# Performance work log

Measured on AMD Instinct MI355X. Metric: run time of the kernel, lower is better.

Reference implementation:

```python
import jax, jax.numpy as jnp
import numpy as np

B = 1024        # batch of clips
MAX_LEN = 14    # temporal length, pinned by spatial_shapes=[[max_len,1]]
D_MODEL = 1024
N_HEADS = 16
N_POINTS = 4
H_SP, W_SP = MAX_LEN, 1  # level-0 spatial shape (H, W)


def setup_inputs() -> dict:
    key = jax.random.key(0)
    ks = jax.random.split(key, 12)
    s = 0.02
    lin = lambda k, i, o: (jax.random.normal(k, (i, o), jnp.float32) * s)
    vec = lambda k, o: (jax.random.normal(k, (o,), jnp.float32) * s)
    return {
        "x": jax.random.normal(ks[0], (B, MAX_LEN, D_MODEL), jnp.float32),
        "W_value": lin(ks[1], D_MODEL, D_MODEL), "b_value": vec(ks[2], D_MODEL),
        "W_off": lin(ks[3], D_MODEL, N_HEADS * N_POINTS * 2), "b_off": vec(ks[4], N_HEADS * N_POINTS * 2),
        "W_attn": lin(ks[5], D_MODEL, N_HEADS * N_POINTS), "b_attn": vec(ks[6], N_HEADS * N_POINTS),
        "W_out": lin(ks[7], D_MODEL, D_MODEL), "b_out": vec(ks[8], D_MODEL),
        "W_proj": lin(ks[9], D_MODEL, D_MODEL), "b_proj": vec(ks[10], D_MODEL),
    }


def _msdeform(x, W_value, b_value, W_off, b_off, W_attn, b_attn, W_out, b_out):
    Bq, T, D = x.shape
    heads, P = N_HEADS, N_POINTS
    hd = D // heads
    # value projection -> [B, heads, N=H*W, hd]
    value = (x @ W_value + b_value).reshape(Bq, T, heads, hd).transpose(0, 2, 1, 3)
    # sampling offsets [B,T,heads,P,2] and softmax attention weights [B,T,heads,P]
    off = (x @ W_off + b_off).reshape(Bq, T, heads, P, 2)
    aw = jax.nn.softmax((x @ W_attn + b_attn).reshape(Bq, T, heads, P), axis=-1)
    # reference points: x-coord = linspace(0,1,T), y-coord = 0
    ref = jnp.linspace(0.0, 1.0, T, dtype=x.dtype)
    ref_pts = jnp.stack([ref, jnp.zeros_like(ref)], axis=-1)  # [T,2]
    norm = jnp.array([W_SP, H_SP], dtype=x.dtype)  # offset_normalizer = (W, H)
    locs = ref_pts[None, :, None, None, :] + off / norm  # [B,T,heads,P,2] in [0,1] coords
    # grid_sample bilinear, align_corners=False, padding_mode='zeros':
    # pixel coord = loc * size - 0.5
    ix = locs[..., 0] * W_SP - 0.5
    iy = locs[..., 1] * H_SP - 0.5
    x0 = jnp.floor(ix); y0 = jnp.floor(iy)
    fx = ix - x0; fy = iy - y0
    x0i = x0.astype(jnp.int32); y0i = y0.astype(jnp.int32)
    out = jnp.zeros((Bq, heads, T * P, hd), x.dtype)
    corners = ((0, 0, (1 - fx) * (1 - fy)), (1, 0, fx * (1 - fy)),
               (0, 1, (1 - fx) * fy), (1, 1, fx * fy))
    for dx, dy, w in corners:
        xx = x0i + dx; yy = y0i + dy
        valid = ((xx >= 0) & (xx < W_SP) & (yy >= 0) & (yy < H_SP)).astype(x.dtype)
        idx = jnp.clip(yy, 0, H_SP - 1) * W_SP + jnp.clip(xx, 0, W_SP - 1)  # [B,T,heads,P]
        idx_t = idx.transpose(0, 2, 1, 3).reshape(Bq, heads, T * P)
        v = jnp.take_along_axis(value, idx_t[..., None], axis=2)  # [B,heads,T*P,hd]
        wt = (w * valid).transpose(0, 2, 1, 3).reshape(Bq, heads, T * P)
        out = out + v * wt[..., None]
    out = out.reshape(Bq, heads, T, P, hd)
    attn = jnp.einsum('bhqpd,bqhp->bqhd', out, aw).reshape(Bq, T, D)
    return attn @ W_out + b_out


def reference(x, W_value, b_value, W_off, b_off, W_attn, b_attn, W_out, b_out, W_proj, b_proj):
    y = _msdeform(x, W_value, b_value, W_off, b_off, W_attn, b_attn, W_out, b_out)
    return y @ W_proj + b_proj
```

## Files before the change

kernel.cpp:

```cpp
#include <hip/hip_runtime.h>
#include <hip/hip_bf16.h>

using bf16 = __hip_bfloat16;
typedef __attribute__((ext_vector_type(8))) short bf16x8;
typedef __attribute__((ext_vector_type(4))) float f32x4;

#define NB   1024
#define TT   14
#define DM   1024
#define ROWS (NB*TT)
#define NCAT 1280

__device__ __forceinline__ unsigned short f2b(float f) {
  union { bf16 h; unsigned short u; } cv; cv.h = __float2bfloat16(f); return cv.u;
}

__device__ __forceinline__ void gload16(const bf16* g, bf16* l) {
  __builtin_amdgcn_global_load_lds((const __attribute__((address_space(1))) void*)g,
                                   (__attribute__((address_space(3))) void*)l, 16, 0, 0);
}

__global__ __launch_bounds__(256) void k_prep_all(
    const float* __restrict__ x_in,
    const float* __restrict__ Wv, const float* __restrict__ Wo,
    const float* __restrict__ Wa, const float* __restrict__ Wproj,
    const float* __restrict__ Wout,
    const float* __restrict__ bv, const float* __restrict__ bo,
    const float* __restrict__ ba, const float* __restrict__ b_out,
    const float* __restrict__ b_proj,
    bf16* __restrict__ x_bf,
    bf16* __restrict__ wcat_t, bf16* __restrict__ wproj_t,
    bf16* __restrict__ wout_b, float* __restrict__ bcat,
    float* __restrict__ bcomb) {
  __shared__ float t[32][33];
  const int x = blockIdx.x, y = blockIdx.y;
  const int lx = threadIdx.x & 31, ly = threadIdx.x >> 5;
  if (y < 72) {
    const float* src; bf16* dst; int base, width;
    if (y < 40) {
      dst = wcat_t;
      int n0 = y * 32;
      if (n0 < 1024)      { src = Wv; base = 0;    width = 1024; }
      else if (n0 < 1152) { src = Wo; base = 1024; width = 128;  }
      else if (n0 < 1216) { src = Wa; base = 1152; width = 64;   }
      else                { src = nullptr; base = 0; width = 1;  }
      int k0 = x * 32, n0b = n0;
#pragma unroll
      for (int r = 0; r < 32; r += 8)
        t[ly + r][lx] = src ? src[(size_t)(k0 + ly + r) * width + (n0b - base + lx)] : 0.0f;
      __syncthreads();
#pragma unroll
      for (int r = 0; r < 32; r += 8)
        dst[(size_t)(n0b + ly + r) * 1024 + (k0 + lx)] = __float2bfloat16(t[lx][ly + r]);
    } else {
      int n0 = (y - 40) * 32, k0 = x * 32;
#pragma unroll
      for (int r = 0; r < 32; r += 8)
        t[ly + r][lx] = Wproj[(size_t)(k0 + ly + r) * 1024 + (n0 + lx)];
      __syncthreads();
#pragma unroll
      for (int r = 0; r < 32; r += 8)
        wproj_t[(size_t)(n0 + ly + r) * 1024 + (k0 + lx)] = __float2bfloat16(t[lx][ly + r]);
    }
  } else if (y < 80) {
    int i0 = ((y - 72) * 32 + x) * 1024 + threadIdx.x;
#pragma unroll
    for (int r = 0; r < 4; ++r) {
      int i = i0 + r * 256;
      float4 v = reinterpret_cast<const float4*>(Wout)[i];
      ushort4 o;
      o.x = f2b(v.x); o.y = f2b(v.y); o.z = f2b(v.z); o.w = f2b(v.w);
      reinterpret_cast<ushort4*>(wout_b)[i] = o;
    }
  } else if (y == 80) {
    if (x < 5) {
      int i = x * 256 + threadIdx.x;
      if (i < NCAT) {
        float v = 0.0f;
        if (i < 1024) v = bv[i];
        else if (i < 1152) v = bo[i - 1024];
        else if (i < 1216) v = ba[i - 1152];
        bcat[i] = v;
      }
    } else if (x < 21) {
      __shared__ float part[4][64];
      int j0 = (x - 5) * 64;
      int jl = threadIdx.x & 63, ip = threadIdx.x >> 6;
      int j = j0 + jl;
      float acc = 0.0f;
      int i0 = ip * 256;
      for (int i = i0; i < i0 + 256; ++i)
        acc = fmaf(b_out[i], Wproj[(size_t)i * 1024 + j], acc);
      part[ip][jl] = acc;
      __syncthreads();
      if (threadIdx.x < 64) {
        int jj = j0 + threadIdx.x;
        bcomb[jj] = part[0][threadIdx.x] + part[1][threadIdx.x] +
                    part[2][threadIdx.x] + part[3][threadIdx.x] + b_proj[jj];
      }
    }
  } else {
    int id = (y - 81) * 32 + x;
    int i0 = id * 2048 + threadIdx.x;
#pragma unroll
    for (int r = 0; r < 8; ++r) {
      int i = i0 + r * 256;
      float4 v = reinterpret_cast<const float4*>(x_in)[i];
      ushort4 o;
      o.x = f2b(v.x); o.y = f2b(v.y); o.z = f2b(v.z); o.w = f2b(v.w);
      reinterpret_cast<ushort4*>(x_bf)[i] = o;
    }
  }
}

template<int OUT1, int OUT2>
__global__ __launch_bounds__(256, 4) void k_gemm_dual(
    const bf16* __restrict__ A1, const bf16* __restrict__ B1,
    void* __restrict__ C1v, const float* __restrict__ bias1,
    int N1, int K1, int lda1, int ldb1, int nx1, int nwg1,
    const bf16* __restrict__ A2, const bf16* __restrict__ B2,
    void* __restrict__ C2v, const float* __restrict__ bias2,
    int N2, int K2, int lda2, int ldb2, int nx2) {
  constexpr int ASZ = 4096, BSZ = 4096;
  __shared__ bf16 As[2 * ASZ];
  __shared__ bf16 Bs[2 * BSZ];

  const int tid  = threadIdx.x;
  const int wave = tid >> 6, lane = tid & 63;

  const bf16 *A, *Bt; void* Cv; const float* bias;
  int N, K, lda, ldb, bx, by; bool ob;
  if ((int)blockIdx.x < nwg1) {
    int bid = blockIdx.x;
    int q = nwg1 >> 3, r = nwg1 & 7;
    int xcd = bid & 7, li = bid >> 3;
    bid = (xcd < r ? xcd * (q + 1) : r * (q + 1) + (xcd - r) * q) + li;
    A = A1; Bt = B1; Cv = C1v; bias = bias1;
    N = N1; K = K1; lda = lda1; ldb = ldb1;
    bx = bid % nx1; by = bid / nx1; ob = (OUT1 != 0);
  } else {
    int bid = blockIdx.x - nwg1;
    A = A2; Bt = B2; Cv = C2v; bias = bias2;
    N = N2; K = K2; lda = lda2; ldb = ldb2;
    bx = bid % nx2; by = bid / nx2; ob = (OUT2 != 0);
  }
  const int row0 = by * 128, col0 = bx * 128;
  const int wr = (wave >> 1) * 64, wc = (wave & 1) * 64;
  f32x4 acc[4][4] = {};

  const int sr  = tid >> 2;
  const int scb = (tid & 3) ^ ((tid >> 3) & 3);
  const bf16* Ab = A  + (size_t)(row0 + sr) * lda + scb * 8;
  const bf16* Bb = Bt + (size_t)(col0 + sr) * ldb + scb * 8;

  const int fr = lane & 15, g = lane >> 4;
  const int fs = (g ^ ((fr >> 1) & 3)) * 8;
  int aoff[4], boff[4];
#pragma unroll
  for (int mi = 0; mi < 4; ++mi) {
    int row = wr + mi * 16 + fr, h = row >> 6, lr = row & 63;
    aoff[mi] = h * 2048 + lr * 32 + fs;
  }
#pragma unroll
  for (int ni = 0; ni < 4; ++ni) {
    int row = wc + ni * 16 + fr, h = row >> 6, lr = row & 63;
    boff[ni] = h * 2048 + lr * 32 + fs;
  }

  auto STAGE = [&](int s, int kk) {
    const int ko = kk * 32;
#pragma unroll
    for (int j = 0; j < 2; ++j)
      gload16(Ab + (size_t)j * 64 * lda + ko, As + s * ASZ + j * 2048 + tid * 8);
#pragma unroll
    for (int j = 0; j < 2; ++j)
      gload16(Bb + (size_t)j * 64 * ldb + ko, Bs + s * BSZ + j * 2048 + tid * 8);
  };
  auto COMPUTE = [&](int s) {
    const bf16* as = As + s * ASZ;
    const bf16* bs = Bs + s * BSZ;
    bf16x8 af[4], bfm[4];
#pragma unroll
    for (int mi = 0; mi < 4; ++mi) af[mi] = *(const bf16x8*)(as + aoff[mi]);
#pragma unroll
    for (int ni = 0; ni < 4; ++ni) bfm[ni] = *(const bf16x8*)(bs + boff[ni]);
    __builtin_amdgcn_s_setprio(1);
#pragma unroll
    for (int mi = 0; mi < 4; ++mi)
#pragma unroll
      for (int ni = 0; ni < 4; ++ni)
        acc[mi][ni] = __builtin_amdgcn_mfma_f32_16x16x32_bf16(bfm[ni], af[mi], acc[mi][ni], 0, 0, 0);
    __builtin_amdgcn_s_setprio(0);
  };

  const int nk = K >> 5;
  STAGE(0, 0);
  STAGE(1, 1);
  int cur = 0;
  for (int i = 0; i < nk; ++i) {
    if (i < nk - 1) asm volatile("s_waitcnt vmcnt(4)" ::: "memory");
    else            asm volatile("s_waitcnt vmcnt(0)" ::: "memory");
    __builtin_amdgcn_s_barrier();
    asm volatile("" ::: "memory");
    COMPUTE(cur);
    __builtin_amdgcn_s_barrier();
    asm volatile("" ::: "memory");
    if (i + 2 < nk) STAGE(cur, i + 2);
    cur ^= 1;
  }

  const int fq = g * 4;
#pragma unroll
  for (int mi = 0; mi < 4; ++mi) {
    int gr = row0 + wr + mi * 16 + fr;
#pragma unroll
    for (int ni = 0; ni < 4; ++ni) {
      int gc = col0 + wc + ni * 16 + fq;
      float b0 = 0, b1 = 0, b2 = 0, b3 = 0;
      if (bias) {
        float4 bv = *reinterpret_cast<const float4*>(bias + gc);
        b0 = bv.x; b1 = bv.y; b2 = bv.z; b3 = bv.w;
      }
      float v0 = acc[mi][ni][0] + b0, v1 = acc[mi][ni][1] + b1;
      float v2 = acc[mi][ni][2] + b2, v3 = acc[mi][ni][3] + b3;
      if (ob) {
        ushort4 u; u.x = f2b(v0); u.y = f2b(v1); u.z = f2b(v2); u.w = f2b(v3);
        *reinterpret_cast<ushort4*>((bf16*)Cv + (size_t)gr * N + gc) = u;
      } else {
        float4 o; o.x = v0; o.y = v1; o.z = v2; o.w = v3;
        *reinterpret_cast<float4*>((float*)Cv + (size_t)gr * N + gc) = o;
      }
    }
  }
}

__global__ __launch_bounds__(512) void k_sample(const bf16* __restrict__ C1,
                                                bf16* __restrict__ y) {
  const int wave = threadIdx.x >> 6, lane = threadIdx.x & 63;
  const int row = blockIdx.x * 8 + wave;
  const int b = row / TT, t = row - b * TT;
  const bf16* r1 = C1 + (size_t)row * NCAT;

  float offx, offy;
  {
    ushort2 u = *reinterpret_cast<const ushort2*>(r1 + 1024 + lane * 2);
    offx = __uint_as_float(((unsigned)u.x) << 16);
    offy = __uint_as_float(((unsigned)u.y) << 16);
  }
  float logit;
  {
    unsigned short u = reinterpret_cast<const unsigned short*>(r1)[1152 + lane];
    logit = __uint_as_float(((unsigned)u) << 16);
  }
  float m = fmaxf(logit, __shfl_xor(logit, 1));
  m = fmaxf(m, __shfl_xor(m, 2));
  float e = __expf(logit - m);
  float s = e + __shfl_xor(e, 1);
  s = s + __shfl_xor(s, 2);
  float aw = e / s;

  const float refx = (float)t * (1.0f / 13.0f);
  float ix = refx + offx - 0.5f;
  float xf = floorf(ix);
  float fx = ix - xf;
  float wx = (xf == 0.0f) ? (1.0f - fx) : ((xf == -1.0f) ? fx : 0.0f);

  float iy = offy - 0.5f;
  float yf = floorf(iy);
  float fy = iy - yf;
  int y0 = (int)yf, y1 = y0 + 1;
  float w0 = (y0 >= 0 && y0 < TT) ? (1.0f - fy) : 0.0f;
  float w1 = (y1 >= 0 && y1 < TT) ? fy : 0.0f;
  int i0 = max(0, min(TT - 1, y0));
  int i1 = max(0, min(TT - 1, y1));
  float cw0 = aw * wx * w0;
  float cw1 = aw * wx * w1;

  const bf16* vb = C1 + (size_t)(b * TT) * NCAT;
  const int hofs = (lane & 32) ? 8 : 0;
  const int cofs = (lane & 31) * 2;
  float acc0[8], acc1[8];
#pragma unroll
  for (int h = 0; h < 8; ++h) { acc0[h] = 0.0f; acc1[h] = 0.0f; }
#pragma unroll
  for (int j = 0; j < 32; ++j) {
    const int src = j + (lane & 32);
    float c0 = __shfl(cw0, src);
    float c1 = __shfl(cw1, src);
    int a0 = __shfl(i0, src);
    int a1 = __shfl(i1, src);
    const int hb = j >> 2;
    const int ho = (hb + hofs) * 64 + cofs;
    ushort2 u0 = *reinterpret_cast<const ushort2*>(
        reinterpret_cast<const unsigned short*>(vb) + (size_t)a0 * NCAT + ho);
    ushort2 u1 = *reinterpret_cast<const ushort2*>(
        reinterpret_cast<const unsigned short*>(vb) + (size_t)a1 * NCAT + ho);
    float v00 = __uint_as_float(((unsigned)u0.x) << 16);
    float v01 = __uint_as_float(((unsigned)u0.y) << 16);
    float v10 = __uint_as_float(((unsigned)u1.x) << 16);
    float v11 = __uint_as_float(((unsigned)u1.y) << 16);
    acc0[hb] = fmaf(c0, v00, fmaf(c1, v10, acc0[hb]));
    acc1[hb] = fmaf(c0, v01, fmaf(c1, v11, acc1[hb]));
  }
#pragma unroll
  for (int hb = 0; hb < 8; ++hb) {
    ushort2 o;
    o.x = f2b(acc0[hb]);
    o.y = f2b(acc1[hb]);
    *reinterpret_cast<ushort2*>(
        reinterpret_cast<unsigned short*>(y) +
        (size_t)row * DM + (hb + hofs) * 64 + cofs) = o;
  }
}

extern "C" void kernel_launch(void* const* d_in, const int* in_sizes, int n_in,
                              void* d_out, int out_size, void* d_ws, size_t ws_size,
                              hipStream_t stream) {
  (void)in_sizes; (void)n_in; (void)out_size; (void)ws_size;
  const float* x       = (const float*)d_in[0];
  const float* W_value = (const float*)d_in[1];
  const float* b_value = (const float*)d_in[2];
  const float* W_off   = (const float*)d_in[3];
  const float* b_off   = (const float*)d_in[4];
  const float* W_attn  = (const float*)d_in[5];
  const float* b_attn  = (const float*)d_in[6];
  const float* W_out   = (const float*)d_in[7];
  const float* b_out   = (const float*)d_in[8];
  const float* W_proj  = (const float*)d_in[9];
  const float* b_proj  = (const float*)d_in[10];

  char* ws = (char*)d_ws;
  bf16*  x_bf    = (bf16*)(ws);
  bf16*  y_bf    = x_bf;
  bf16*  C1      = (bf16*)(ws + 29360128);
  bf16*  Wcat_t  = (bf16*)(ws + 66060288);
  float* bcat    = (float*)(ws + 68681728);
  bf16*  Wout_b  = (bf16*)(ws + 68686848);
  bf16*  Wproj_t = (bf16*)(ws + 70784000);
  bf16*  Wc_t    = (bf16*)(ws + 72881152);
  float* bcomb   = (float*)(ws + 74978304);

  k_prep_all<<<dim3(32, 137), 256, 0, stream>>>(
      x, W_value, W_off, W_attn, W_proj, W_out,
      b_value, b_off, b_attn, b_out, b_proj,
      x_bf, Wcat_t, Wproj_t, Wout_b, bcat, bcomb);

  k_gemm_dual<1, 1><<<1120 + 64, 256, 0, stream>>>(
      x_bf, Wcat_t, C1, bcat, NCAT, DM, DM, DM, NCAT / 128, 1120,
      Wproj_t, Wout_b, Wc_t, nullptr, 1024, 1024, 1024, 1024, 8);

  k_sample<<<ROWS / 8, 512, 0, stream>>>(C1, y_bf);

  k_gemm_dual<0, 0><<<896, 256, 0, stream>>>(
      y_bf, Wc_t, (float*)d_out, bcomb, DM, DM, DM, DM, DM / 128, 896,
      y_bf, Wc_t, (float*)d_out, bcomb, DM, DM, DM, DM, DM / 128);
}
```

Before: 156.6 us.

## Replace final GEMM with 256x256-tile 8-wave kernel using quadrant-pipelined LDS loads

```diff
diff --git a/kernel.cpp b/kernel.cpp
--- a/kernel.cpp
+++ b/kernel.cpp
@@ -234,6 +234,157 @@
   }
 }
 
+template<int HAS_BIAS>
+__global__ __launch_bounds__(512, 1) void k_gemm8q(
+    const bf16* __restrict__ A, const bf16* __restrict__ Bt,
+    float* __restrict__ C, const float* __restrict__ bias,
+    int N, int K, int lda, int ldb, int nx) {
+  __shared__ bf16 As[2][2][8192];
+  __shared__ bf16 Bs[2][2][8192];
+  const int tid = threadIdx.x, w = tid >> 6, l = tid & 63;
+  const int wm = w >> 2, wn = w & 3;
+
+  int bid = blockIdx.x;
+  { int nwg = gridDim.x; int q = nwg >> 3, r = nwg & 7;
+    int xcd = bid & 7, li = bid >> 3;
+    bid = (xcd < r ? xcd * (q + 1) : r * (q + 1) + (xcd - r) * q) + li; }
+  const int bx = bid % nx, by = bid / nx;
+  const int row0 = by * 256, col0 = bx * 256;
+
+  const int srow  = tid >> 3;
+  const int sslot = ((tid & 7) ^ ((tid >> 3) & 7)) * 8;
+  const bf16* Ag = A  + (size_t)(row0 + srow) * lda + sslot;
+  const bf16* Bg = Bt + (size_t)(col0 + srow) * ldb + sslot;
+
+  const int fr = l & 15, g = l >> 4;
+  const int fs0 = (g ^ (fr & 7)) * 8;
+  const int fs1 = ((4 + g) ^ (fr & 7)) * 8;
+
+  f32x4 acc[8][4] = {};
+
+#define SA8(d, hh, t) { \
+    gload16(Ag + (size_t)((hh) * 128) * lda + (t) * 64,      &As[d][hh][tid * 8]); \
+    gload16(Ag + (size_t)((hh) * 128 + 64) * lda + (t) * 64, &As[d][hh][4096 + tid * 8]); }
+#define SB8(d, hh, t) { \
+    gload16(Bg + (size_t)((hh) * 128) * ldb + (t) * 64,      &Bs[d][hh][tid * 8]); \
+    gload16(Bg + (size_t)((hh) * 128 + 64) * ldb + (t) * 64, &Bs[d][hh][4096 + tid * 8]); }
+
+#define RD8(d, qm, qn) \
+    const bf16* ah = &As[d][wm][(qm) * 4096]; \
+    const bf16* bh = &Bs[d][wn >> 1][(wn & 1) * 4096 + (qn) * 2048]; \
+    bf16x8 af[4][2], bv[2][2]; \
+    _Pragma("unroll") for (int mi = 0; mi < 4; ++mi) { int ro = (mi * 16 + fr) * 64; \
+      af[mi][0] = *(const bf16x8*)(ah + ro + fs0); \
+      af[mi][1] = *(const bf16x8*)(ah + ro + fs1); } \
+    _Pragma("unroll") for (int nj = 0; nj < 2; ++nj) { int ro = (nj * 16 + fr) * 64; \
+      bv[nj][0] = *(const bf16x8*)(bh + ro + fs0); \
+      bv[nj][1] = *(const bf16x8*)(bh + ro + fs1); }
+
+#define MM8(qm, qn) \
+    __builtin_amdgcn_s_setprio(1); \
+    _Pragma("unroll") for (int mi = 0; mi < 4; ++mi) \
+      _Pragma("unroll") for (int nj = 0; nj < 2; ++nj) { \
+        acc[(qm)*4+mi][(qn)*2+nj] = __builtin_amdgcn_mfma_f32_16x16x32_bf16( \
+            bv[nj][0], af[mi][0], acc[(qm)*4+mi][(qn)*2+nj], 0, 0, 0); \
+        acc[(qm)*4+mi][(qn)*2+nj] = __builtin_amdgcn_mfma_f32_16x16x32_bf16( \
+            bv[nj][1], af[mi][1], acc[(qm)*4+mi][(qn)*2+nj], 0, 0, 0); } \
+    __builtin_amdgcn_s_setprio(0);
+
+#define LGKM0 \
+    asm volatile("s_waitcnt lgkmcnt(0)" ::: "memory"); \
+    __builtin_amdgcn_sched_barrier(0);
+
+  const int nt = K >> 6, ni = nt >> 1;
+  SA8(0, 0, 0) SA8(0, 1, 0) SB8(0, 0, 0) SB8(0, 1, 0)
+
+  for (int j = 0; j < ni; ++j) {
+    const int v = 2 * j + 1, w2 = 2 * j + 2;
+    const bool pw = (w2 < nt);
+    { SA8(1, 0, v)
+      asm volatile("s_waitcnt vmcnt(2)" ::: "memory");
+      __builtin_amdgcn_s_barrier();
+      RD8(0, 0, 0)
+      LGKM0
+      MM8(0, 0)
+      __builtin_amdgcn_s_barrier();
+      asm volatile("" ::: "memory"); }
+    { RD8(0, 0, 1)
+      SA8(1, 1, v)
+      __builtin_amdgcn_s_barrier();
+      LGKM0
+      MM8(0, 1)
+      __builtin_amdgcn_s_barrier();
+      asm volatile("" ::: "memory"); }
+    { RD8(0, 1, 0)
+      SB8(1, 0, v)
+      __builtin_amdgcn_s_barrier();
+      LGKM0
+      MM8(1, 0)
+      __builtin_amdgcn_s_barrier();
+      asm volatile("" ::: "memory"); }
+    { RD8(0, 1, 1)
+      SB8(1, 1, v)
+      __builtin_amdgcn_s_barrier();
+      LGKM0
+      MM8(1, 1)
+      __builtin_amdgcn_s_barrier();
+      asm volatile("" ::: "memory"); }
+    { if (pw) SA8(0, 0, w2)
+      if (pw) { asm volatile("s_waitcnt vmcnt(2)" ::: "memory"); }
+      else    { asm volatile("s_waitcnt vmcnt(0)" ::: "memory"); }
+      __builtin_amdgcn_s_barrier();
+      RD8(1, 0, 0)
+      LGKM0
+      MM8(0, 0)
+      __builtin_amdgcn_s_barrier();
+      asm volatile("" ::: "memory"); }
+    { RD8(1, 0, 1)
+      if (pw) SA8(0, 1, w2)
+      __builtin_amdgcn_s_barrier();
+      LGKM0
+      MM8(0, 1)
+      __builtin_amdgcn_s_barrier();
+      asm volatile("" ::: "memory"); }
+    { RD8(1, 1, 0)
+      if (pw) SB8(0, 0, w2)
+      __builtin_amdgcn_s_barrier();
+      LGKM0
+      MM8(1, 0)
+      __builtin_amdgcn_s_barrier();
+      asm volatile("" ::: "memory"); }
+    { RD8(1, 1, 1)
+      if (pw) SB8(0, 1, w2)
+      __builtin_amdgcn_s_barrier();
+      LGKM0
+      MM8(1, 1)
+      __builtin_amdgcn_s_barrier();
+      asm volatile("" ::: "memory"); }
+  }
+
+#pragma unroll
+  for (int m = 0; m < 8; ++m) {
+    int gr = row0 + wm * 128 + (m >> 2) * 64 + (m & 3) * 16 + fr;
+#pragma unroll
+    for (int n = 0; n < 4; ++n) {
+      int gc = col0 + wn * 64 + (n >> 1) * 32 + (n & 1) * 16 + g * 4;
+      float b0 = 0, b1 = 0, b2 = 0, b3 = 0;
+      if (HAS_BIAS) {
+        float4 bb = *reinterpret_cast<const float4*>(bias + gc);
+        b0 = bb.x; b1 = bb.y; b2 = bb.z; b3 = bb.w;
+      }
+      float4 o;
+      o.x = acc[m][n][0] + b0; o.y = acc[m][n][1] + b1;
+      o.z = acc[m][n][2] + b2; o.w = acc[m][n][3] + b3;
+      *reinterpret_cast<float4*>(C + (size_t)gr * N + gc) = o;
+    }
+  }
+#undef SA8
+#undef SB8
+#undef RD8
+#undef MM8
+#undef LGKM0
+}
+
 __global__ __launch_bounds__(512) void k_sample(const bf16* __restrict__ C1,
                                                 bf16* __restrict__ y) {
   const int wave = threadIdx.x >> 6, lane = threadIdx.x & 63;
@@ -351,7 +502,6 @@
 
   k_sample<<<ROWS / 8, 512, 0, stream>>>(C1, y_bf);
 
-  k_gemm_dual<0, 0><<<896, 256, 0, stream>>>(
-      y_bf, Wc_t, (float*)d_out, bcomb, DM, DM, DM, DM, DM / 128, 896,
-      y_bf, Wc_t, (float*)d_out, bcomb, DM, DM, DM, DM, DM / 128);
-}
+  k_gemm8q<1><<<224, 512, 0, stream>>>(
+      y_bf, Wc_t, (float*)d_out, bcomb, DM, DM, DM, DM, 4);
+}
```

Measured after the change: 156.4 us. Within noise of the previous version (-0.1%).
